# Optimization experiments

Hardware: AMD Instinct MI355X
Metric: run time of the kernel (lower is better)

Reference implementation:

```python
import jax, jax.numpy as jnp
import numpy as np

SIGMA = 5.0
THRESH = 0.1

def setup_inputs() -> dict:
    key = jax.random.key(0)
    k1, k2, k3 = jax.random.split(key, 3)
    B, N, H, W = 8, 20, 512, 512
    y_pred = jax.random.normal(k1, (B, 1, H, W), dtype=jnp.float32)
    point_labels = jax.random.randint(k2, (B, N), 0, 2, dtype=jnp.int32)
    point_coords = jax.random.uniform(k3, (B, N, 2), dtype=jnp.float32)
    return {"y_pred": y_pred, "point_labels": point_labels, "point_coords": point_coords}


def _soft_labels(point_labels, point_coords, H, W):
    # Replicates the sequential overwrite-scatter: for each pixel, the LAST
    B, N = point_labels.shape
    yc = point_coords[..., 0] * H  # (B, N)
    xc = point_coords[..., 1] * W  # (B, N)
    yg = jnp.arange(H, dtype=jnp.float32)
    xg = jnp.arange(W, dtype=jnp.float32)
    # (B, N, H, W) squared distance from each point to each pixel
    dist_sq = (yg[None, None, :, None] - yc[:, :, None, None]) ** 2 \
            + (xg[None, None, None, :] - xc[:, :, None, None]) ** 2
    mask = jnp.exp(-dist_sq / (2.0 * SIGMA ** 2)) > THRESH  # (B, N, H, W)
    n_idx = jnp.arange(N, dtype=jnp.int32)[None, :, None, None]
    last = jnp.max(jnp.where(mask, n_idx, -1), axis=1)  # (B, H, W); -1 = no point
    valid = last >= 0
    labels = jnp.take_along_axis(
        point_labels.astype(jnp.float32)[:, :, None], last.clip(0).reshape(B, 1, -1)[:, 0][:, None, :].swapaxes(1, 2)[..., 0][:, None, :], axis=1
    ) if False else point_labels.astype(jnp.float32)[jnp.arange(B)[:, None, None], last.clip(0)]
    return labels, valid


def reference(y_pred, point_labels, point_coords):
    B, _, H, W = y_pred.shape
    labels, valid = _soft_labels(point_labels, point_coords, H, W)
    logits = y_pred[:, 0]  # (B, H, W)
    # numerically-stable BCE with logits
    bce = jnp.maximum(logits, 0.0) - logits * labels + jnp.log1p(jnp.exp(-jnp.abs(logits)))
    cnt = valid.sum()
    loss = jnp.where(cnt > 0,
                     jnp.sum(bce * valid) / jnp.maximum(cnt, 1).astype(jnp.float32),
                     jnp.float32(0.0))
    return loss
```

## Files before the change

### kernel.cpp

```cpp
#include <hip/hip_runtime.h>
#include <math.h>


#define R2_THRESH 115.12925464970229f
#define HW 512
#define NPTS 20
#define ROWS_PER_BLOCK 8
#define NBLOCKS 512
#define MAGIC 0x5F3C9A17u

__global__ __launch_bounds__(256)
void pce_one_kernel(const float* __restrict__ y_pred,
                    const int* __restrict__ point_labels,
                    const float* __restrict__ point_coords,
                    float* __restrict__ ws,
                    unsigned* __restrict__ flags,
                    float* __restrict__ out) {
    const int b     = blockIdx.x >> 6;
    const int chunk = blockIdx.x & 63;
    const int y0    = chunk * ROWS_PER_BLOCK;
    const int tid   = threadIdx.x;
    const int r     = tid >> 5;
    const int lane  = tid & 31;

    __shared__ float s_xc[ROWS_PER_BLOCK][NPTS];
    __shared__ float s_lim[ROWS_PER_BLOCK][NPTS];
    __shared__ float s_lab[ROWS_PER_BLOCK][NPTS];

    float xlo = INFINITY, xhi = -INFINITY;
    if (lane < NPTS) {
        const int n = lane;
        float yc  = point_coords[b * (NPTS * 2) + n * 2 + 0] * (float)HW;
        float xc  = point_coords[b * (NPTS * 2) + n * 2 + 1] * (float)HW;
        float dy  = (float)(y0 + r) - yc;
        float lim = R2_THRESH - dy * dy;
        s_xc[r][n]  = xc;
        s_lim[r][n] = lim;
        s_lab[r][n] = (float)point_labels[b * NPTS + n];
        if (lim > 0.0f) {
            float s = sqrtf(lim);
            xlo = xc - s;
            xhi = xc + s;
        }
    }
    #pragma unroll
    for (int off = 16; off > 0; off >>= 1) {
        xlo = fminf(xlo, __shfl_xor(xlo, off, 32));
        xhi = fmaxf(xhi, __shfl_xor(xhi, off, 32));
    }
    const int x0 = (int)fminf(fmaxf(floorf(xlo), 0.0f), 512.0f);
    const int x1 = (int)fminf(fmaxf(ceilf(xhi), -1.0f), 511.0f);
    __syncthreads();

    float sum = 0.0f, cnt = 0.0f;
    const float* row = y_pred + (size_t)b * HW * HW + (size_t)(y0 + r) * HW;
    for (int px = x0 + lane; px <= x1; px += 32) {
        const float fx = (float)px;
        float lab = 0.0f;
        bool  valid = false;
        #pragma unroll
        for (int k = 0; k < NPTS; ++k) {
            float dx = fx - s_xc[r][k];
            if (dx * dx < s_lim[r][k]) { lab = s_lab[r][k]; valid = true; }
        }
        if (valid) {
            float l   = row[px];
            float bce = fmaxf(l, 0.0f) - l * lab + log1pf(expf(-fabsf(l)));
            sum += bce;
            cnt += 1.0f;
        }
    }

    #pragma unroll
    for (int off = 32; off > 0; off >>= 1) {
        sum += __shfl_down(sum, off, 64);
        cnt += __shfl_down(cnt, off, 64);
    }
    __shared__ float rs[4], rc[4];
    if ((tid & 63) == 0) { rs[tid >> 6] = sum; rc[tid >> 6] = cnt; }
    __syncthreads();
    if (tid == 0) {
        float S = rs[0] + rs[1] + rs[2] + rs[3];
        float C = rc[0] + rc[1] + rc[2] + rc[3];
        __hip_atomic_store(&ws[blockIdx.x * 2 + 0], S, __ATOMIC_RELAXED, __HIP_MEMORY_SCOPE_AGENT);
        __hip_atomic_store(&ws[blockIdx.x * 2 + 1], C, __ATOMIC_RELAXED, __HIP_MEMORY_SCOPE_AGENT);
        __hip_atomic_store(&flags[blockIdx.x], MAGIC, __ATOMIC_RELEASE, __HIP_MEMORY_SCOPE_AGENT);
    }
    if (blockIdx.x != 0) return;

    {
        unsigned f1 = 0, f2 = 0;
        while (f1 != MAGIC || f2 != MAGIC) {
            if (f1 != MAGIC)
                f1 = __hip_atomic_load(&flags[tid],       __ATOMIC_ACQUIRE, __HIP_MEMORY_SCOPE_AGENT);
            if (f2 != MAGIC)
                f2 = __hip_atomic_load(&flags[tid + 256], __ATOMIC_ACQUIRE, __HIP_MEMORY_SCOPE_AGENT);
            if (f1 != MAGIC || f2 != MAGIC) __builtin_amdgcn_s_sleep(1);
        }
    }
    __syncthreads();

    {
        float Sa = __hip_atomic_load(&ws[tid * 2 + 0],         __ATOMIC_RELAXED, __HIP_MEMORY_SCOPE_AGENT);
        float Ca = __hip_atomic_load(&ws[tid * 2 + 1],         __ATOMIC_RELAXED, __HIP_MEMORY_SCOPE_AGENT);
        float Sb = __hip_atomic_load(&ws[(tid + 256) * 2 + 0], __ATOMIC_RELAXED, __HIP_MEMORY_SCOPE_AGENT);
        float Cb = __hip_atomic_load(&ws[(tid + 256) * 2 + 1], __ATOMIC_RELAXED, __HIP_MEMORY_SCOPE_AGENT);
        float S = Sa + Sb;
        float C = Ca + Cb;
        #pragma unroll
        for (int off = 32; off > 0; off >>= 1) {
            S += __shfl_down(S, off, 64);
            C += __shfl_down(C, off, 64);
        }
        __shared__ float fs[4], fc[4];
        if ((tid & 63) == 0) { fs[tid >> 6] = S; fc[tid >> 6] = C; }
        __syncthreads();
        if (tid == 0) {
            float SS = fs[0] + fs[1] + fs[2] + fs[3];
            float CC = fc[0] + fc[1] + fc[2] + fc[3];
            out[0] = (CC > 0.0f) ? (SS / CC) : 0.0f;
        }
        __syncthreads();
        __hip_atomic_store(&flags[tid],       0u, __ATOMIC_RELAXED, __HIP_MEMORY_SCOPE_AGENT);
        __hip_atomic_store(&flags[tid + 256], 0u, __ATOMIC_RELAXED, __HIP_MEMORY_SCOPE_AGENT);
    }
}

extern "C" void kernel_launch(void* const* d_in, const int* in_sizes, int n_in,
                              void* d_out, int out_size, void* d_ws, size_t ws_size,
                              hipStream_t stream) {
    const float* y_pred       = (const float*)d_in[0];
    const int*   point_labels = (const int*)d_in[1];
    const float* point_coords = (const float*)d_in[2];
    float*       out          = (float*)d_out;
    float*       ws           = (float*)d_ws;
    unsigned*    flags        = (unsigned*)((float*)d_ws + 1024);

    pce_one_kernel<<<NBLOCKS, 256, 0, stream>>>(y_pred, point_labels, point_coords,
                                                ws, flags, out);
}
```

Before: 21.06 us.

## Use 64 blocks of 64 rows each and finish the reduction in one wavefront

Drops the grid from 512 blocks of 8 rows to 64 blocks that each loop over 64 rows in 8 groups, precomputing per-row x ranges in shared memory. The final cross-block reduction now polls only 63 flags and reduces them within a single wavefront, with no shared-memory stage or extra barriers. The aim is to cut launch and last-block serialization overhead, since the real work is sparse. The cost is less parallelism: fewer CUs are busy, and each block does more serial work.

```diff
diff --git a/kernel.cpp b/kernel.cpp
--- a/kernel.cpp
+++ b/kernel.cpp
@@ -5,8 +5,8 @@
 #define R2_THRESH 115.12925464970229f
 #define HW 512
 #define NPTS 20
-#define ROWS_PER_BLOCK 8
-#define NBLOCKS 512
+#define ROWS_PER_CHUNK 64
+#define NBLOCKS 64
 #define MAGIC 0x5F3C9A17u
 
 __global__ __launch_bounds__(256)
@@ -16,58 +16,74 @@
                     float* __restrict__ ws,
                     unsigned* __restrict__ flags,
                     float* __restrict__ out) {
-    const int b     = blockIdx.x >> 6;
-    const int chunk = blockIdx.x & 63;
-    const int y0    = chunk * ROWS_PER_BLOCK;
+    const int b     = blockIdx.x >> 3;
+    const int chunk = blockIdx.x & 7;
+    const int y0    = chunk * ROWS_PER_CHUNK;
     const int tid   = threadIdx.x;
-    const int r     = tid >> 5;
+    const int r8    = tid >> 5;
     const int lane  = tid & 31;
 
-    __shared__ float s_xc[ROWS_PER_BLOCK][NPTS];
-    __shared__ float s_lim[ROWS_PER_BLOCK][NPTS];
-    __shared__ float s_lab[ROWS_PER_BLOCK][NPTS];
+    __shared__ float s_xc[ROWS_PER_CHUNK][NPTS];
+    __shared__ float s_lim[ROWS_PER_CHUNK][NPTS];
+    __shared__ float s_lab[ROWS_PER_CHUNK][NPTS];
+    __shared__ int   s_x0[ROWS_PER_CHUNK], s_x1[ROWS_PER_CHUNK];
 
-    float xlo = INFINITY, xhi = -INFINITY;
+    float yc = 0.0f, xc = 0.0f, lab = 0.0f;
     if (lane < NPTS) {
-        const int n = lane;
-        float yc  = point_coords[b * (NPTS * 2) + n * 2 + 0] * (float)HW;
-        float xc  = point_coords[b * (NPTS * 2) + n * 2 + 1] * (float)HW;
-        float dy  = (float)(y0 + r) - yc;
-        float lim = R2_THRESH - dy * dy;
-        s_xc[r][n]  = xc;
-        s_lim[r][n] = lim;
-        s_lab[r][n] = (float)point_labels[b * NPTS + n];
-        if (lim > 0.0f) {
-            float s = sqrtf(lim);
-            xlo = xc - s;
-            xhi = xc + s;
+        yc  = point_coords[b * (NPTS * 2) + lane * 2 + 0] * (float)HW;
+        xc  = point_coords[b * (NPTS * 2) + lane * 2 + 1] * (float)HW;
+        lab = (float)point_labels[b * NPTS + lane];
+    }
+
+    #pragma unroll
+    for (int g = 0; g < 8; ++g) {
+        const int row = g * 8 + r8;
+        float xlo = INFINITY, xhi = -INFINITY;
+        if (lane < NPTS) {
+            float dy  = (float)(y0 + row) - yc;
+            float lim = R2_THRESH - dy * dy;
+            s_xc[row][lane]  = xc;
+            s_lim[row][lane] = lim;
+            s_lab[row][lane] = lab;
+            if (lim > 0.0f) {
+                float s = sqrtf(lim);
+                xlo = xc - s;
+                xhi = xc + s;
+            }
+        }
+        #pragma unroll
+        for (int off = 16; off > 0; off >>= 1) {
+            xlo = fminf(xlo, __shfl_xor(xlo, off, 32));
+            xhi = fmaxf(xhi, __shfl_xor(xhi, off, 32));
+        }
+        if (lane == 0) {
+            s_x0[row] = (int)fminf(fmaxf(floorf(xlo), 0.0f), 512.0f);
+            s_x1[row] = (int)fminf(fmaxf(ceilf(xhi), -1.0f), 511.0f);
         }
     }
-    #pragma unroll
-    for (int off = 16; off > 0; off >>= 1) {
-        xlo = fminf(xlo, __shfl_xor(xlo, off, 32));
-        xhi = fmaxf(xhi, __shfl_xor(xhi, off, 32));
-    }
-    const int x0 = (int)fminf(fmaxf(floorf(xlo), 0.0f), 512.0f);
-    const int x1 = (int)fminf(fmaxf(ceilf(xhi), -1.0f), 511.0f);
     __syncthreads();
 
     float sum = 0.0f, cnt = 0.0f;
-    const float* row = y_pred + (size_t)b * HW * HW + (size_t)(y0 + r) * HW;
-    for (int px = x0 + lane; px <= x1; px += 32) {
-        const float fx = (float)px;
-        float lab = 0.0f;
-        bool  valid = false;
-        #pragma unroll
-        for (int k = 0; k < NPTS; ++k) {
-            float dx = fx - s_xc[r][k];
-            if (dx * dx < s_lim[r][k]) { lab = s_lab[r][k]; valid = true; }
-        }
-        if (valid) {
-            float l   = row[px];
-            float bce = fmaxf(l, 0.0f) - l * lab + log1pf(expf(-fabsf(l)));
-            sum += bce;
-            cnt += 1.0f;
+    const float* base = y_pred + (size_t)b * HW * HW;
+    for (int g = 0; g < 8; ++g) {
+        const int row = g * 8 + r8;
+        const int x0 = s_x0[row], x1 = s_x1[row];
+        const float* rp = base + (size_t)(y0 + row) * HW;
+        for (int px = x0 + lane; px <= x1; px += 32) {
+            const float fx = (float)px;
+            float pl = 0.0f;
+            bool  valid = false;
+            #pragma unroll
+            for (int k = 0; k < NPTS; ++k) {
+                float dx = fx - s_xc[row][k];
+                if (dx * dx < s_lim[row][k]) { pl = s_lab[row][k]; valid = true; }
+            }
+            if (valid) {
+                float l   = rp[px];
+                float bce = fmaxf(l, 0.0f) - l * pl + log1pf(expf(-fabsf(l)));
+                sum += bce;
+                cnt += 1.0f;
+            }
         }
     }
 
@@ -84,45 +100,26 @@
         float C = rc[0] + rc[1] + rc[2] + rc[3];
         __hip_atomic_store(&ws[blockIdx.x * 2 + 0], S, __ATOMIC_RELAXED, __HIP_MEMORY_SCOPE_AGENT);
         __hip_atomic_store(&ws[blockIdx.x * 2 + 1], C, __ATOMIC_RELAXED, __HIP_MEMORY_SCOPE_AGENT);
-        __hip_atomic_store(&flags[blockIdx.x], MAGIC, __ATOMIC_RELEASE, __HIP_MEMORY_SCOPE_AGENT);
+        if (blockIdx.x != 0)
+            __hip_atomic_store(&flags[blockIdx.x], MAGIC, __ATOMIC_RELEASE, __HIP_MEMORY_SCOPE_AGENT);
     }
     if (blockIdx.x != 0) return;
 
-    {
-        unsigned f1 = 0, f2 = 0;
-        while (f1 != MAGIC || f2 != MAGIC) {
-            if (f1 != MAGIC)
-                f1 = __hip_atomic_load(&flags[tid],       __ATOMIC_ACQUIRE, __HIP_MEMORY_SCOPE_AGENT);
-            if (f2 != MAGIC)
-                f2 = __hip_atomic_load(&flags[tid + 256], __ATOMIC_ACQUIRE, __HIP_MEMORY_SCOPE_AGENT);
-            if (f1 != MAGIC || f2 != MAGIC) __builtin_amdgcn_s_sleep(1);
+    if (tid < 64) {
+        if (tid >= 1) {
+            unsigned f = 0;
+            while (f != MAGIC)
+                f = __hip_atomic_load(&flags[tid], __ATOMIC_ACQUIRE, __HIP_MEMORY_SCOPE_AGENT);
         }
-    }
-    __syncthreads();
-
-    {
-        float Sa = __hip_atomic_load(&ws[tid * 2 + 0],         __ATOMIC_RELAXED, __HIP_MEMORY_SCOPE_AGENT);
-        float Ca = __hip_atomic_load(&ws[tid * 2 + 1],         __ATOMIC_RELAXED, __HIP_MEMORY_SCOPE_AGENT);
-        float Sb = __hip_atomic_load(&ws[(tid + 256) * 2 + 0], __ATOMIC_RELAXED, __HIP_MEMORY_SCOPE_AGENT);
-        float Cb = __hip_atomic_load(&ws[(tid + 256) * 2 + 1], __ATOMIC_RELAXED, __HIP_MEMORY_SCOPE_AGENT);
-        float S = Sa + Sb;
-        float C = Ca + Cb;
+        float S = __hip_atomic_load(&ws[tid * 2 + 0], __ATOMIC_RELAXED, __HIP_MEMORY_SCOPE_AGENT);
+        float C = __hip_atomic_load(&ws[tid * 2 + 1], __ATOMIC_RELAXED, __HIP_MEMORY_SCOPE_AGENT);
         #pragma unroll
         for (int off = 32; off > 0; off >>= 1) {
             S += __shfl_down(S, off, 64);
             C += __shfl_down(C, off, 64);
         }
-        __shared__ float fs[4], fc[4];
-        if ((tid & 63) == 0) { fs[tid >> 6] = S; fc[tid >> 6] = C; }
-        __syncthreads();
-        if (tid == 0) {
-            float SS = fs[0] + fs[1] + fs[2] + fs[3];
-            float CC = fc[0] + fc[1] + fc[2] + fc[3];
-            out[0] = (CC > 0.0f) ? (SS / CC) : 0.0f;
-        }
-        __syncthreads();
-        __hip_atomic_store(&flags[tid],       0u, __ATOMIC_RELAXED, __HIP_MEMORY_SCOPE_AGENT);
-        __hip_atomic_store(&flags[tid + 256], 0u, __ATOMIC_RELAXED, __HIP_MEMORY_SCOPE_AGENT);
+        if (tid == 0) out[0] = (C > 0.0f) ? (S / C) : 0.0f;
+        __hip_atomic_store(&flags[tid], 0u, __ATOMIC_RELAXED, __HIP_MEMORY_SCOPE_AGENT);
     }
 }
 
@@ -134,7 +131,7 @@
     const float* point_coords = (const float*)d_in[2];
     float*       out          = (float*)d_out;
     float*       ws           = (float*)d_ws;
-    unsigned*    flags        = (unsigned*)((float*)d_ws + 1024);
+    unsigned*    flags        = (unsigned*)((float*)d_ws + 128);
 
     pce_one_kernel<<<NBLOCKS, 256, 0, stream>>>(y_pred, point_labels, point_coords,
                                                 ws, flags, out);
```

After: 45.77 us. +117.4%, slower.
